# Optimization experiments

Hardware: AMD Instinct MI355X
Metric: run time of the kernel (lower is better)

The kernel has to match this reference:

```python
import jax, jax.numpy as jnp
import numpy as np

N = 50000
E = 800000
NFEAT = 128
HID = 64
EPS = 1e-5


def setup_inputs() -> dict:
    key = jax.random.key(0)
    ks = jax.random.split(key, 12)
    def xavier(k, fi, fo):
        lim = float(np.sqrt(6.0 / (fi + fo)))
        return jax.random.uniform(k, (fi, fo), jnp.float32, -lim, lim)
    return {
        "x": jax.random.normal(ks[0], (N, NFEAT), jnp.float32),
        "edge_index": jax.random.randint(ks[1], (2, E), 0, N),
        "W0": xavier(ks[2], NFEAT, HID), "b0": jnp.zeros((HID,), jnp.float32),
        "W1": xavier(ks[3], HID, HID),   "b1": jnp.zeros((HID,), jnp.float32),
        "W2": xavier(ks[4], HID, HID),   "b2": jnp.zeros((HID,), jnp.float32),
        "g0": jnp.ones((HID,), jnp.float32), "be0": jnp.zeros((HID,), jnp.float32),
        "g1": jnp.ones((HID,), jnp.float32), "be1": jnp.zeros((HID,), jnp.float32),
        "fcW": xavier(ks[5], HID, 1), "fcb": jnp.zeros((1,), jnp.float32),
    }


def _gcn_conv(h, src, dst, norm, W, b):
    # h: [N, Fin] -> transform then normalized scatter-add over edges (incl. self loops)
    m = (h @ W)[src] * norm[:, None]            # [E+N, Fout]
    return jax.ops.segment_sum(m, dst, num_segments=N) + b


def _batchnorm(h, g, b):
    mu = jnp.mean(h, axis=0)
    var = jnp.mean((h - mu) ** 2, axis=0)       # biased var, as torch BN
    return (h - mu) * jax.lax.rsqrt(var + EPS) * g + b


def reference(x, edge_index, W0, b0, W1, b1, W2, b2, g0, be0, g1, be1, fcW, fcb):
    loops = jnp.arange(N)
    src = jnp.concatenate([edge_index[0], loops])
    dst = jnp.concatenate([edge_index[1], loops])
    deg = jax.ops.segment_sum(jnp.ones_like(dst, jnp.float32), dst, num_segments=N)
    dinv = jnp.where(deg > 0, jax.lax.rsqrt(jnp.maximum(deg, 1.0)), 0.0)
    norm = dinv[src] * dinv[dst]                # symmetric GCN normalization

    h = x  # dropout is identity in eval
    h = jax.nn.relu(_batchnorm(_gcn_conv(h, src, dst, norm, W0, b0), g0, be0))
    h = jax.nn.relu(_batchnorm(_gcn_conv(h, src, dst, norm, W1, b1), g1, be1))
    h = jax.nn.relu(_gcn_conv(h, src, dst, norm, W2, b2))
    return (h @ fcW + fcb).squeeze(-1)          # [N]
```

## Files before the change

kernel.cpp:

```cpp
#include <hip/hip_runtime.h>

#define N_NODES 50000
#define N_EDGES 800000
#define NFEAT   128
#define HID     64
#define EPS_BN  1e-5f
#define NCHUNK  2
#define CHN     (N_NODES / NCHUNK)
#define SENT    50000

#define NPB     256
#define NCBIN   196
#define BPB     (NPB * NCHUNK)
#define EPBLK   2048
#define NB1     ((N_EDGES + EPBLK - 1) / EPBLK)
#define MAXPAD  (3 * BPB + 4)

#define NBINS   64
#define NBLKN   ((N_NODES + 255) / 256)
#define NPAIR   (N_NODES / 2)

typedef unsigned int   u32x4 __attribute__((ext_vector_type(4)));
typedef unsigned short u16x4 __attribute__((ext_vector_type(4)));

__device__ __forceinline__ float u2f_lo(unsigned int u) {
    union { unsigned int i; float f; } c; c.i = u << 16; return c.f;
}
__device__ __forceinline__ float u2f_hi(unsigned int u) {
    union { unsigned int i; float f; } c; c.i = u & 0xffff0000u; return c.f;
}
__device__ __forceinline__ float b2f(unsigned short u) {
    union { unsigned int i; float f; } c; c.i = ((unsigned int)u) << 16; return c.f;
}
__device__ __forceinline__ unsigned int f2b2(float lo, float hi) {
    union { float f; unsigned int i; } a, b;
    a.f = lo; b.f = hi;
    unsigned int x = (a.i + 0x7fffu + ((a.i >> 16) & 1u)) >> 16;
    unsigned int y = (b.i + 0x7fffu + ((b.i >> 16) & 1u)) & 0xffff0000u;
    return x | y;
}

__global__ void k_zero(float* __restrict__ st0, float* __restrict__ st1,
                       unsigned short* __restrict__ ts,
                       unsigned short* __restrict__ sent) {
    int i = threadIdx.x;
    if (i < 2 * HID) { st0[i] = 0.f; st1[i] = 0.f; }
    if (i < 32) ((unsigned int*)(ts + (size_t)N_NODES * HID))[i] = 0u;
    if (i < 4) sent[i] = SENT;
}

__global__ __launch_bounds__(256) void k_p1(const int* __restrict__ ei,
                                            unsigned int* __restrict__ packed,
                                            unsigned short* __restrict__ lrankE,
                                            int* __restrict__ bhE) {
    __shared__ int h[NCBIN];
    const int tid = threadIdx.x;
    for (int i = tid; i < NCBIN; i += 256) h[i] = 0;
    __syncthreads();
    const int base = blockIdx.x * EPBLK;
#pragma unroll
    for (int it = 0; it < EPBLK / 256; ++it) {
        int e = base + it * 256 + tid;
        if (e < N_EDGES) {
            unsigned s = (unsigned)ei[e];
            unsigned t = (unsigned)ei[N_EDGES + e];
            packed[e] = (t << 16) | s;
            lrankE[e] = (unsigned short)atomicAdd(&h[t >> 8], 1);
        }
    }
    __syncthreads();
    for (int i = tid; i < NCBIN; i += 256) bhE[i * NB1 + blockIdx.x] = h[i];
}

__global__ __launch_bounds__(512) void k_p1scan(int* __restrict__ bhE,
                                                int* __restrict__ bintotE) {
    const int b = blockIdx.x, tid = threadIdx.x;
    int v = (tid < NB1) ? bhE[b * NB1 + tid] : 0;
    __shared__ int sm[512];
    sm[tid] = v;
    __syncthreads();
    for (int off = 1; off < 512; off <<= 1) {
        int t = (tid >= off) ? sm[tid - off] : 0;
        __syncthreads();
        sm[tid] += t;
        __syncthreads();
    }
    if (tid < NB1) bhE[b * NB1 + tid] = sm[tid] - v;
    if (tid == 511) bintotE[b] = sm[511];
}

__global__ void k_binbase(const int* __restrict__ bintotE, int* __restrict__ binbase) {
    const int tid = threadIdx.x;
    int v = (tid < NCBIN) ? bintotE[tid] : 0;
    __shared__ int sm[256];
    sm[tid] = v;
    __syncthreads();
    for (int off = 1; off < 256; off <<= 1) {
        int t = (tid >= off) ? sm[tid - off] : 0;
        __syncthreads();
        sm[tid] += t;
        __syncthreads();
    }
    if (tid < NCBIN) binbase[tid] = sm[tid] - v;
    if (tid == NCBIN - 1) binbase[NCBIN] = sm[tid];
}

__global__ __launch_bounds__(256) void k_p3(const unsigned int* __restrict__ packed,
                                            const unsigned short* __restrict__ lrankE,
                                            const int* __restrict__ bhE,
                                            const int* __restrict__ binbase,
                                            unsigned int* __restrict__ binned) {
    const int base = blockIdx.x * EPBLK;
#pragma unroll
    for (int it = 0; it < EPBLK / 256; ++it) {
        int e = base + it * 256 + threadIdx.x;
        if (e < N_EDGES) {
            unsigned p = packed[e];
            int bin = (int)(p >> 24);
            int pos = binbase[bin] + bhE[bin * NB1 + blockIdx.x] + lrankE[e];
            binned[pos] = p;
        }
    }
}

__global__ __launch_bounds__(256) void k_p4(const unsigned int* __restrict__ binned,
                                            const int* __restrict__ binbase,
                                            unsigned short* __restrict__ col,
                                            int2* __restrict__ nspan,
                                            float* __restrict__ dinv) {
    __shared__ int cnt[BPB];
    __shared__ int lrp[BPB];
    __shared__ int fillc[BPB];
    __shared__ int scanTmp[256];
    const int bin = blockIdx.x, tid = threadIdx.x;
    const int e0 = binbase[bin], e1 = binbase[bin + 1];
    const int t0 = bin * NPB;
    for (int i = tid; i < BPB; i += 256) { cnt[i] = 0; fillc[i] = 0; }
    __syncthreads();
    for (int i = e0 + tid; i < e1; i += 256) {
        unsigned p = binned[i];
        int t = (int)(p >> 16), s = (int)(p & 0xffffu);
        int lb = ((t - t0) << 1) | (s >= CHN);
        atomicAdd(&cnt[lb], 1);
    }
    __syncthreads();
    const int p0 = (cnt[2 * tid] + 3) & ~3;
    const int p1 = (cnt[2 * tid + 1] + 3) & ~3;
    const int mysum = p0 + p1;
    scanTmp[tid] = mysum;
    __syncthreads();
    for (int off = 1; off < 256; off <<= 1) {
        int t = (tid >= off) ? scanTmp[tid - off] : 0;
        __syncthreads();
        scanTmp[tid] += t;
        __syncthreads();
    }
    const int pre = scanTmp[tid] - mysum;
    lrp[2 * tid]     = pre;
    lrp[2 * tid + 1] = pre + p0;
    const int colbase = ((e0 + 3) & ~3) + bin * MAXPAD;
    {
        const int node = t0 + tid;
        if (node < N_NODES) {
            int st = colbase + pre;
            nspan[node] = make_int2(st, st + p0 + p1);
            dinv[node] = rsqrtf((float)(cnt[2 * tid] + cnt[2 * tid + 1] + 1));
        }
    }
    __syncthreads();
    for (int i = e0 + tid; i < e1; i += 256) {
        unsigned p = binned[i];
        int t = (int)(p >> 16), s = (int)(p & 0xffffu);
        int lb = ((t - t0) << 1) | (s >= CHN);
        int pos = colbase + lrp[lb] + atomicAdd(&fillc[lb], 1);
        col[pos] = (unsigned short)s;
    }
    __syncthreads();
    for (int lb = tid; lb < BPB; lb += 256) {
        int c = cnt[lb];
        int pc = (c + 3) & ~3;
        int b2 = colbase + lrp[lb];
        for (int q = c; q < pc; ++q) col[b2 + q] = SENT;
    }
}

__device__ __forceinline__ int node_bin2(const int2* __restrict__ nspan, int i) {
    int iters = (nspan[i].y - nspan[i].x) >> 2;
    if (iters > NBINS - 1) iters = NBINS - 1;
    return (NBINS - 1) - iters;
}

__global__ __launch_bounds__(256) void k_hist2(const int2* __restrict__ nspan,
                                               int* __restrict__ bhistS,
                                               int* __restrict__ lrankS) {
    __shared__ int h[NBINS];
    const int tid = threadIdx.x;
    if (tid < NBINS) h[tid] = 0;
    __syncthreads();
    const int i = blockIdx.x * 256 + tid;
    if (i < N_NODES) lrankS[i] = atomicAdd(&h[node_bin2(nspan, i)], 1);
    __syncthreads();
    if (tid < NBINS) bhistS[tid * NBLKN + blockIdx.x] = h[tid];
}

__global__ __launch_bounds__(256) void k_colscan(int* __restrict__ bhistS,
                                                 int* __restrict__ bintotS) {
    const int b = blockIdx.x, tid = threadIdx.x;
    int v = (tid < NBLKN) ? bhistS[b * NBLKN + tid] : 0;
    __shared__ int sm[256];
    sm[tid] = v;
    __syncthreads();
    for (int off = 1; off < 256; off <<= 1) {
        int t = (tid >= off) ? sm[tid - off] : 0;
        __syncthreads();
        sm[tid] += t;
        __syncthreads();
    }
    if (tid < NBLKN) bhistS[b * NBLKN + tid] = sm[tid] - v;
    if (tid == 255) bintotS[b] = sm[255];
}

__global__ void k_binscan(const int* __restrict__ bintotS, int* __restrict__ binoffS) {
    int tid = threadIdx.x;
    int v = (tid < NBINS) ? bintotS[tid] : 0;
    int s = v;
#pragma unroll
    for (int off = 1; off < 64; off <<= 1) {
        int t = __shfl_up(s, off, 64);
        if (tid >= off) s += t;
    }
    if (tid < NBINS) binoffS[tid] = s - v;
}

__global__ __launch_bounds__(256) void k_sortscatter(const int2* __restrict__ nspan,
                                                     const int* __restrict__ binoffS,
                                                     const int* __restrict__ bhistS,
                                                     const int* __restrict__ lrankS,
                                                     int* __restrict__ perm,
                                                     int2* __restrict__ span) {
    int i = blockIdx.x * 256 + threadIdx.x;
    if (i >= N_NODES) return;
    int b = node_bin2(nspan, i);
    int pos = binoffS[b] + bhistS[b * NBLKN + blockIdx.x] + lrankS[i];
    perm[pos] = i;
    span[pos] = nspan[i];
}

template <int K, bool AFFINE, bool HBF16>
__global__ __launch_bounds__(256) void k_gemm(const void* __restrict__ Hv,
                                              const float* __restrict__ W,
                                              const float* __restrict__ dinv,
                                              const float* __restrict__ affine,
                                              unsigned short* __restrict__ ts) {
    __shared__ float Ws[K * HID];
    __shared__ float As[2 * K];
    const int tid = threadIdx.x;
    for (int i = tid * 4; i < K * HID; i += 256 * 4)
        *(float4*)&Ws[i] = *(const float4*)&W[i];
    if (AFFINE) {
        if (tid < (2 * K) / 4)
            *(float4*)&As[tid * 4] = *(const float4*)&affine[tid * 4];
    }
    __syncthreads();

    const int quad = tid & 3;
    const int rp_  = tid >> 2;
    const int row  = blockIdx.x * 128 + rp_ * 2;
    const int c0   = quad * 16;
    const bool v0  = row < N_NODES;
    const bool v1  = row + 1 < N_NODES;

    float acc0[16], acc1[16];
#pragma unroll
    for (int i = 0; i < 16; ++i) { acc0[i] = 0.f; acc1[i] = 0.f; }

    const float*          h0f = (const float*)Hv + (size_t)row * K;
    const unsigned short* h0b = (const unsigned short*)Hv + (size_t)row * K;
    const float4 z4 = make_float4(0.f, 0.f, 0.f, 0.f);

#pragma unroll 2
    for (int k = 0; k < K; k += 4) {
        float4 ha, hb;
        if constexpr (HBF16) {
            ushort4 ua = v0 ? *(const ushort4*)(h0b + k)     : make_ushort4(0, 0, 0, 0);
            ushort4 ub = v1 ? *(const ushort4*)(h0b + K + k) : make_ushort4(0, 0, 0, 0);
            ha = make_float4(b2f(ua.x), b2f(ua.y), b2f(ua.z), b2f(ua.w));
            hb = make_float4(b2f(ub.x), b2f(ub.y), b2f(ub.z), b2f(ub.w));
        } else {
            ha = v0 ? *(const float4*)(h0f + k)     : z4;
            hb = v1 ? *(const float4*)(h0f + K + k) : z4;
        }
        if (AFFINE) {
            const float4 sc = *(const float4*)&As[k];
            const float4 sh = *(const float4*)&As[K + k];
            ha.x = fmaxf(0.f, fmaf(ha.x, sc.x, sh.x));
            ha.y = fmaxf(0.f, fmaf(ha.y, sc.y, sh.y));
            ha.z = fmaxf(0.f, fmaf(ha.z, sc.z, sh.z));
            ha.w = fmaxf(0.f, fmaf(ha.w, sc.w, sh.w));
            hb.x = fmaxf(0.f, fmaf(hb.x, sc.x, sh.x));
            hb.y = fmaxf(0.f, fmaf(hb.y, sc.y, sh.y));
            hb.z = fmaxf(0.f, fmaf(hb.z, sc.z, sh.z));
            hb.w = fmaxf(0.f, fmaf(hb.w, sc.w, sh.w));
        }
        const float hA[4] = { ha.x, ha.y, ha.z, ha.w };
        const float hB[4] = { hb.x, hb.y, hb.z, hb.w };
#pragma unroll
        for (int j = 0; j < 4; ++j) {
            const float4* wr = (const float4*)&Ws[(k + j) * HID + c0];
            const float xa = hA[j], xb = hB[j];
#pragma unroll
            for (int q = 0; q < 4; ++q) {
                const float4 wv = wr[q];
                acc0[q * 4 + 0] = fmaf(xa, wv.x, acc0[q * 4 + 0]);
                acc0[q * 4 + 1] = fmaf(xa, wv.y, acc0[q * 4 + 1]);
                acc0[q * 4 + 2] = fmaf(xa, wv.z, acc0[q * 4 + 2]);
                acc0[q * 4 + 3] = fmaf(xa, wv.w, acc0[q * 4 + 3]);
                acc1[q * 4 + 0] = fmaf(xb, wv.x, acc1[q * 4 + 0]);
                acc1[q * 4 + 1] = fmaf(xb, wv.y, acc1[q * 4 + 1]);
                acc1[q * 4 + 2] = fmaf(xb, wv.z, acc1[q * 4 + 2]);
                acc1[q * 4 + 3] = fmaf(xb, wv.w, acc1[q * 4 + 3]);
            }
        }
    }

    if (v0) {
        const float d = dinv[row];
        uint4 p0, p1;
        p0.x = f2b2(acc0[0] * d,  acc0[1] * d);
        p0.y = f2b2(acc0[2] * d,  acc0[3] * d);
        p0.z = f2b2(acc0[4] * d,  acc0[5] * d);
        p0.w = f2b2(acc0[6] * d,  acc0[7] * d);
        p1.x = f2b2(acc0[8] * d,  acc0[9] * d);
        p1.y = f2b2(acc0[10] * d, acc0[11] * d);
        p1.z = f2b2(acc0[12] * d, acc0[13] * d);
        p1.w = f2b2(acc0[14] * d, acc0[15] * d);
        uint4* dst = (uint4*)&ts[(size_t)row * HID + c0];
        dst[0] = p0; dst[1] = p1;
    }
    if (v1) {
        const float d = dinv[row + 1];
        uint4 p0, p1;
        p0.x = f2b2(acc1[0] * d,  acc1[1] * d);
        p0.y = f2b2(acc1[2] * d,  acc1[3] * d);
        p0.z = f2b2(acc1[4] * d,  acc1[5] * d);
        p0.w = f2b2(acc1[6] * d,  acc1[7] * d);
        p1.x = f2b2(acc1[8] * d,  acc1[9] * d);
        p1.y = f2b2(acc1[10] * d, acc1[11] * d);
        p1.z = f2b2(acc1[12] * d, acc1[13] * d);
        p1.w = f2b2(acc1[14] * d, acc1[15] * d);
        uint4* dst = (uint4*)&ts[(size_t)(row + 1) * HID + c0];
        dst[0] = p0; dst[1] = p1;
    }
}

#define ACC8A(r)                                            \
    a0 += u2f_lo(r.x); a1 += u2f_hi(r.x);                   \
    a2 += u2f_lo(r.y); a3 += u2f_hi(r.y);                   \
    a4 += u2f_lo(r.z); a5 += u2f_hi(r.z);                   \
    a6 += u2f_lo(r.w); a7 += u2f_hi(r.w);
#define ACC8B(r)                                            \
    b0 += u2f_lo(r.x); b1 += u2f_hi(r.x);                   \
    b2 += u2f_lo(r.y); b3 += u2f_hi(r.y);                   \
    b4 += u2f_lo(r.z); b5 += u2f_hi(r.z);                   \
    b6 += u2f_lo(r.w); b7 += u2f_hi(r.w);

#define GATHER_PAIR(sA, sB)                                                     \
    {                                                                           \
        int eA = sA.x, eB = sB.x;                                               \
        const int endA = sA.y, endB = sB.y;                                     \
        const int lenA = endA - eA, lenB = endB - eB;                           \
        const int iters = (lenA > lenB ? lenA : lenB) >> 2;                     \
        u16x4 cA = __builtin_nontemporal_load((eA < endA) ? (const u16x4*)&col[eA] : (const u16x4*)sent4); \
        u16x4 cB = __builtin_nontemporal_load((eB < endB) ? (const u16x4*)&col[eB] : (const u16x4*)sent4); \
        for (int it = 0; it < iters; ++it) {                                    \
            eA += 4; eB += 4;                                                   \
            const u16x4 nA = __builtin_nontemporal_load((eA < endA) ? (const u16x4*)&col[eA] : (const u16x4*)sent4); \
            const u16x4 nB = __builtin_nontemporal_load((eB < endB) ? (const u16x4*)&col[eB] : (const u16x4*)sent4); \
            const uint4 rA0 = ts8[(size_t)cA.x * 8 + sl];                       \
            const uint4 rA1 = ts8[(size_t)cA.y * 8 + sl];                       \
            const uint4 rA2 = ts8[(size_t)cA.z * 8 + sl];                       \
            const uint4 rA3 = ts8[(size_t)cA.w * 8 + sl];                       \
            const uint4 rB0 = ts8[(size_t)cB.x * 8 + sl];                       \
            const uint4 rB1 = ts8[(size_t)cB.y * 8 + sl];                       \
            const uint4 rB2 = ts8[(size_t)cB.z * 8 + sl];                       \
            const uint4 rB3 = ts8[(size_t)cB.w * 8 + sl];                       \
            ACC8A(rA0) ACC8A(rA1) ACC8A(rA2) ACC8A(rA3)                         \
            ACC8B(rB0) ACC8B(rB1) ACC8B(rB2) ACC8B(rB3)                         \
            cA = nA; cB = nB;                                                   \
        }                                                                       \
    }

__global__ __launch_bounds__(256) void k_gather_bn(const uint4* __restrict__ ts8,
                                                   const int* __restrict__ perm,
                                                   const int2* __restrict__ span,
                                                   const unsigned short* __restrict__ col,
                                                   const unsigned short* __restrict__ sent4,
                                                   const float* __restrict__ dinv,
                                                   const float* __restrict__ bias,
                                                   unsigned short* __restrict__ y,
                                                   float* __restrict__ stats) {
    const int tid  = threadIdx.x;
    const int w    = tid >> 6;
    const int lane = tid & 63;
    const int grp  = lane >> 3;
    const int sl   = lane & 7;
    const float4 bv0 = ((const float4*)bias)[2 * sl];
    const float4 bv1 = ((const float4*)bias)[2 * sl + 1];
    float s0=0.f,s1=0.f,s2=0.f,s3=0.f,s4=0.f,s5=0.f,s6=0.f,s7=0.f;
    float q0=0.f,q1=0.f,q2=0.f,q3=0.f,q4=0.f,q5=0.f,q6=0.f,q7=0.f;

    for (int p = blockIdx.x * 32 + w * 8 + grp; p < NPAIR; p += gridDim.x * 32) {
        const int idxA = p;
        const int idxB = N_NODES - 1 - p;
        const int nodeA = perm[idxA];
        const int nodeB = perm[idxB];
        const int2 sA = span[idxA];
        const int2 sB = span[idxB];
        const uint4 selfA = ts8[(size_t)nodeA * 8 + sl];
        const uint4 selfB = ts8[(size_t)nodeB * 8 + sl];
        float a0 = u2f_lo(selfA.x), a1 = u2f_hi(selfA.x);
        float a2 = u2f_lo(selfA.y), a3 = u2f_hi(selfA.y);
        float a4 = u2f_lo(selfA.z), a5 = u2f_hi(selfA.z);
        float a6 = u2f_lo(selfA.w), a7 = u2f_hi(selfA.w);
        float b0 = u2f_lo(selfB.x), b1 = u2f_hi(selfB.x);
        float b2 = u2f_lo(selfB.y), b3 = u2f_hi(selfB.y);
        float b4 = u2f_lo(selfB.z), b5 = u2f_hi(selfB.z);
        float b6 = u2f_lo(selfB.w), b7 = u2f_hi(selfB.w);

        GATHER_PAIR(sA, sB)

        const float dA = dinv[nodeA];
        const float dB = dinv[nodeB];
        const float vA0 = fmaf(a0, dA, bv0.x), vA1 = fmaf(a1, dA, bv0.y);
        const float vA2 = fmaf(a2, dA, bv0.z), vA3 = fmaf(a3, dA, bv0.w);
        const float vA4 = fmaf(a4, dA, bv1.x), vA5 = fmaf(a5, dA, bv1.y);
        const float vA6 = fmaf(a6, dA, bv1.z), vA7 = fmaf(a7, dA, bv1.w);
        const float vB0 = fmaf(b0, dB, bv0.x), vB1 = fmaf(b1, dB, bv0.y);
        const float vB2 = fmaf(b2, dB, bv0.z), vB3 = fmaf(b3, dB, bv0.w);
        const float vB4 = fmaf(b4, dB, bv1.x), vB5 = fmaf(b5, dB, bv1.y);
        const float vB6 = fmaf(b6, dB, bv1.z), vB7 = fmaf(b7, dB, bv1.w);
        u32x4 yA, yB;
        yA.x = f2b2(vA0, vA1); yA.y = f2b2(vA2, vA3);
        yA.z = f2b2(vA4, vA5); yA.w = f2b2(vA6, vA7);
        yB.x = f2b2(vB0, vB1); yB.y = f2b2(vB2, vB3);
        yB.z = f2b2(vB4, vB5); yB.w = f2b2(vB6, vB7);
        __builtin_nontemporal_store(yA, (u32x4*)(y + (size_t)nodeA * HID + sl * 8));
        __builtin_nontemporal_store(yB, (u32x4*)(y + (size_t)nodeB * HID + sl * 8));
        s0 += vA0 + vB0; q0 += vA0 * vA0 + vB0 * vB0;
        s1 += vA1 + vB1; q1 += vA1 * vA1 + vB1 * vB1;
        s2 += vA2 + vB2; q2 += vA2 * vA2 + vB2 * vB2;
        s3 += vA3 + vB3; q3 += vA3 * vA3 + vB3 * vB3;
        s4 += vA4 + vB4; q4 += vA4 * vA4 + vB4 * vB4;
        s5 += vA5 + vB5; q5 += vA5 * vA5 + vB5 * vB5;
        s6 += vA6 + vB6; q6 += vA6 * vA6 + vB6 * vB6;
        s7 += vA7 + vB7; q7 += vA7 * vA7 + vB7 * vB7;
    }

#pragma unroll
    for (int off = 8; off <= 32; off <<= 1) {
        s0 += __shfl_xor(s0, off, 64); q0 += __shfl_xor(q0, off, 64);
        s1 += __shfl_xor(s1, off, 64); q1 += __shfl_xor(q1, off, 64);
        s2 += __shfl_xor(s2, off, 64); q2 += __shfl_xor(q2, off, 64);
        s3 += __shfl_xor(s3, off, 64); q3 += __shfl_xor(q3, off, 64);
        s4 += __shfl_xor(s4, off, 64); q4 += __shfl_xor(q4, off, 64);
        s5 += __shfl_xor(s5, off, 64); q5 += __shfl_xor(q5, off, 64);
        s6 += __shfl_xor(s6, off, 64); q6 += __shfl_xor(q6, off, 64);
        s7 += __shfl_xor(s7, off, 64); q7 += __shfl_xor(q7, off, 64);
    }
    __shared__ float smS[4][64];
    __shared__ float smQ[4][64];
    if (grp == 0) {
        *(float4*)&smS[w][8 * sl]     = make_float4(s0, s1, s2, s3);
        *(float4*)&smS[w][8 * sl + 4] = make_float4(s4, s5, s6, s7);
        *(float4*)&smQ[w][8 * sl]     = make_float4(q0, q1, q2, q3);
        *(float4*)&smQ[w][8 * sl + 4] = make_float4(q4, q5, q6, q7);
    }
    __syncthreads();
    if (tid < 64) {
        float t1 = smS[0][tid] + smS[1][tid] + smS[2][tid] + smS[3][tid];
        float t2 = smQ[0][tid] + smQ[1][tid] + smQ[2][tid] + smQ[3][tid];
        atomicAdd(&stats[tid],      t1);
        atomicAdd(&stats[64 + tid], t2);
    }
}

__global__ void k_bn_final(const float* __restrict__ stats,
                           const float* __restrict__ g,
                           const float* __restrict__ be,
                           float* __restrict__ affine) {
    int c = threadIdx.x;
    if (c < HID) {
        float mu  = stats[c] * (1.0f / N_NODES);
        float var = stats[64 + c] * (1.0f / N_NODES) - mu * mu;
        var = fmaxf(var, 0.f);
        float sc = g[c] * rsqrtf(var + EPS_BN);
        affine[c]       = sc;
        affine[HID + c] = fmaf(-mu, sc, be[c]);
    }
}

__global__ __launch_bounds__(256) void k_gather_final(const uint4* __restrict__ ts8,
                                                      const int* __restrict__ perm,
                                                      const int2* __restrict__ span,
                                                      const unsigned short* __restrict__ col,
                                                      const unsigned short* __restrict__ sent4,
                                                      const float* __restrict__ dinv,
                                                      const float* __restrict__ bias2,
                                                      const float* __restrict__ fcW,
                                                      const float* __restrict__ fcb,
                                                      float* __restrict__ out) {
    const int tid  = threadIdx.x;
    const int w    = tid >> 6;
    const int lane = tid & 63;
    const int grp  = lane >> 3;
    const int sl   = lane & 7;
    const float4 bv0 = ((const float4*)bias2)[2 * sl];
    const float4 bv1 = ((const float4*)bias2)[2 * sl + 1];
    const float4 fw0 = ((const float4*)fcW)[2 * sl];
    const float4 fw1 = ((const float4*)fcW)[2 * sl + 1];
    const float  fb  = fcb[0];

    for (int p = blockIdx.x * 32 + w * 8 + grp; p < NPAIR; p += gridDim.x * 32) {
        const int idxA = p;
        const int idxB = N_NODES - 1 - p;
        const int nodeA = perm[idxA];
        const int nodeB = perm[idxB];
        const int2 sA = span[idxA];
        const int2 sB = span[idxB];
        const uint4 selfA = ts8[(size_t)nodeA * 8 + sl];
        const uint4 selfB = ts8[(size_t)nodeB * 8 + sl];
        float a0 = u2f_lo(selfA.x), a1 = u2f_hi(selfA.x);
        float a2 = u2f_lo(selfA.y), a3 = u2f_hi(selfA.y);
        float a4 = u2f_lo(selfA.z), a5 = u2f_hi(selfA.z);
        float a6 = u2f_lo(selfA.w), a7 = u2f_hi(selfA.w);
        float b0 = u2f_lo(selfB.x), b1 = u2f_hi(selfB.x);
        float b2 = u2f_lo(selfB.y), b3 = u2f_hi(selfB.y);
        float b4 = u2f_lo(selfB.z), b5 = u2f_hi(selfB.z);
        float b6 = u2f_lo(selfB.w), b7 = u2f_hi(selfB.w);

        GATHER_PAIR(sA, sB)

        const float dA = dinv[nodeA];
        const float dB = dinv[nodeB];
        float vA = fmaxf(0.f, fmaf(a0, dA, bv0.x)) * fw0.x
                 + fmaxf(0.f, fmaf(a1, dA, bv0.y)) * fw0.y
                 + fmaxf(0.f, fmaf(a2, dA, bv0.z)) * fw0.z
                 + fmaxf(0.f, fmaf(a3, dA, bv0.w)) * fw0.w
                 + fmaxf(0.f, fmaf(a4, dA, bv1.x)) * fw1.x
                 + fmaxf(0.f, fmaf(a5, dA, bv1.y)) * fw1.y
                 + fmaxf(0.f, fmaf(a6, dA, bv1.z)) * fw1.z
                 + fmaxf(0.f, fmaf(a7, dA, bv1.w)) * fw1.w;
        float vB = fmaxf(0.f, fmaf(b0, dB, bv0.x)) * fw0.x
                 + fmaxf(0.f, fmaf(b1, dB, bv0.y)) * fw0.y
                 + fmaxf(0.f, fmaf(b2, dB, bv0.z)) * fw0.z
                 + fmaxf(0.f, fmaf(b3, dB, bv0.w)) * fw0.w
                 + fmaxf(0.f, fmaf(b4, dB, bv1.x)) * fw1.x
                 + fmaxf(0.f, fmaf(b5, dB, bv1.y)) * fw1.y
                 + fmaxf(0.f, fmaf(b6, dB, bv1.z)) * fw1.z
                 + fmaxf(0.f, fmaf(b7, dB, bv1.w)) * fw1.w;
#pragma unroll
        for (int off = 4; off >= 1; off >>= 1) {
            vA += __shfl_xor(vA, off, 64);
            vB += __shfl_xor(vB, off, 64);
        }
        if (sl == 0) {
            out[nodeA] = vA + fb;
            out[nodeB] = vB + fb;
        }
    }
}

extern "C" void kernel_launch(void* const* d_in, const int* in_sizes, int n_in,
                              void* d_out, int out_size, void* d_ws, size_t ws_size,
                              hipStream_t stream) {
    const float* x    = (const float*)d_in[0];
    const int*   ei   = (const int*)d_in[1];
    const float* W0   = (const float*)d_in[2];
    const float* b0   = (const float*)d_in[3];
    const float* W1   = (const float*)d_in[4];
    const float* b1   = (const float*)d_in[5];
    const float* W2   = (const float*)d_in[6];
    const float* b2   = (const float*)d_in[7];
    const float* g0   = (const float*)d_in[8];
    const float* be0  = (const float*)d_in[9];
    const float* g1   = (const float*)d_in[10];
    const float* be1  = (const float*)d_in[11];
    const float* fcW  = (const float*)d_in[12];
    const float* fcb  = (const float*)d_in[13];
    float* out        = (float*)d_out;

    char* ws = (char*)d_ws;
    size_t off = 0;
    auto alloc = [&](size_t bytes) -> void* {
        size_t o = off;
        off += (bytes + 255) & ~(size_t)255;
        return (void*)(ws + o);
    };
    unsigned short* ts   = (unsigned short*)alloc((size_t)(N_NODES + 1) * HID * 2);
    unsigned short* bufY = (unsigned short*)alloc((size_t)N_NODES * HID * 2);
    unsigned short* col  = (unsigned short*)alloc((size_t)(N_EDGES + NCBIN * MAXPAD + 16) * 2);
    unsigned int* packed = (unsigned int*)alloc((size_t)N_EDGES * 4);
    unsigned int* binned = (unsigned int*)alloc((size_t)N_EDGES * 4);
    unsigned short* lrankE = (unsigned short*)alloc((size_t)N_EDGES * 2);
    int*   bhE     = (int*)  alloc((size_t)NCBIN * NB1 * 4);
    int*   bintotE = (int*)  alloc((size_t)NCBIN * 4);
    int*   binbase = (int*)  alloc((size_t)(NCBIN + 1) * 4);
    int2*  nspan   = (int2*) alloc((size_t)N_NODES * 8);
    float* dinv    = (float*)alloc((size_t)N_NODES * 4);
    int*   perm    = (int*)  alloc((size_t)N_NODES * 4);
    int2*  span    = (int2*) alloc((size_t)N_NODES * 8);
    int*   lrankS  = (int*)  alloc((size_t)N_NODES * 4);
    int*   bhistS  = (int*)  alloc((size_t)NBINS * NBLKN * 4);
    int*   bintotS = (int*)  alloc((size_t)NBINS * 4);
    int*   binoffS = (int*)  alloc((size_t)NBINS * 4);
    unsigned short* sent = (unsigned short*)alloc(16);
    float* stats0  = (float*)alloc(2 * HID * 4);
    float* stats1  = (float*)alloc(2 * HID * 4);
    float* affine0 = (float*)alloc(2 * HID * 4);
    float* affine1 = (float*)alloc(2 * HID * 4);

    const int gGemm = (N_NODES + 127) / 128;
    const int gGath = (NPAIR + 31) / 32;

    k_zero<<<1, 256, 0, stream>>>(stats0, stats1, ts, sent);
    k_p1<<<NB1, 256, 0, stream>>>(ei, packed, lrankE, bhE);
    k_p1scan<<<NCBIN, 512, 0, stream>>>(bhE, bintotE);
    k_binbase<<<1, 256, 0, stream>>>(bintotE, binbase);
    k_p3<<<NB1, 256, 0, stream>>>(packed, lrankE, bhE, binbase, binned);
    k_p4<<<NCBIN, 256, 0, stream>>>(binned, binbase, col, nspan, dinv);
    k_hist2<<<NBLKN, 256, 0, stream>>>(nspan, bhistS, lrankS);
    k_colscan<<<NBINS, 256, 0, stream>>>(bhistS, bintotS);
    k_binscan<<<1, 64, 0, stream>>>(bintotS, binoffS);
    k_sortscatter<<<NBLKN, 256, 0, stream>>>(nspan, binoffS, bhistS, lrankS, perm, span);

    k_gemm<NFEAT, false, false><<<gGemm, 256, 0, stream>>>(x, W0, dinv, nullptr, ts);
    k_gather_bn<<<gGath, 256, 0, stream>>>((const uint4*)ts, perm, span, col, sent, dinv, b0, bufY, stats0);
    k_bn_final<<<1, 64, 0, stream>>>(stats0, g0, be0, affine0);

    k_gemm<HID, true, true><<<gGemm, 256, 0, stream>>>(bufY, W1, dinv, affine0, ts);
    k_gather_bn<<<gGath, 256, 0, stream>>>((const uint4*)ts, perm, span, col, sent, dinv, b1, bufY, stats1);
    k_bn_final<<<1, 64, 0, stream>>>(stats1, g1, be1, affine1);

    k_gemm<HID, true, true><<<gGemm, 256, 0, stream>>>(bufY, W2, dinv, affine1, ts);
    k_gather_final<<<gGath, 256, 0, stream>>>((const uint4*)ts, perm, span, col, sent, dinv, b2, fcW, fcb, out);
}
```

Measured before the change: 206.2 us.

## Split feature table into two 32-column planes and gather each half separately

The GEMM output table is stored as two separate bf16 planes of 32 features each, and every gather kernel runs twice, once per plane, with 8-byte loads instead of 16-byte loads. Each plane is half the size of the full table, so the randomly gathered working set is more likely to stay resident in cache. The cost is reading the edge column indices and spans twice and doubling the gather launches, and the final layer now does a read-modify-write on the output.

```diff
diff --git a/kernel.cpp b/kernel.cpp
--- a/kernel.cpp
+++ b/kernel.cpp
@@ -21,6 +21,7 @@
 #define NPAIR   (N_NODES / 2)
 
 typedef unsigned int   u32x4 __attribute__((ext_vector_type(4)));
+typedef unsigned int   u32x2 __attribute__((ext_vector_type(2)));
 typedef unsigned short u16x4 __attribute__((ext_vector_type(4)));
 
 __device__ __forceinline__ float u2f_lo(unsigned int u) {
@@ -41,11 +42,13 @@
 }
 
 __global__ void k_zero(float* __restrict__ st0, float* __restrict__ st1,
-                       unsigned short* __restrict__ ts,
+                       unsigned short* __restrict__ ts0,
+                       unsigned short* __restrict__ ts1,
                        unsigned short* __restrict__ sent) {
     int i = threadIdx.x;
     if (i < 2 * HID) { st0[i] = 0.f; st1[i] = 0.f; }
-    if (i < 32) ((unsigned int*)(ts + (size_t)N_NODES * HID))[i] = 0u;
+    if (i < 16) ((unsigned int*)(ts0 + (size_t)SENT * 32))[i] = 0u;
+    if (i < 16) ((unsigned int*)(ts1 + (size_t)SENT * 32))[i] = 0u;
     if (i < 4) sent[i] = SENT;
 }
 
@@ -251,7 +254,8 @@
                                               const float* __restrict__ W,
                                               const float* __restrict__ dinv,
                                               const float* __restrict__ affine,
-                                              unsigned short* __restrict__ ts) {
+                                              unsigned short* __restrict__ ts0,
+                                              unsigned short* __restrict__ ts1) {
     __shared__ float Ws[K * HID];
     __shared__ float As[2 * K];
     const int tid = threadIdx.x;
@@ -323,6 +327,8 @@
         }
     }
 
+    unsigned short* plane = (c0 < 32) ? ts0 : ts1;
+    const int pc0 = c0 & 31;
     if (v0) {
         const float d = dinv[row];
         uint4 p0, p1;
@@ -334,7 +340,7 @@
         p1.y = f2b2(acc0[10] * d, acc0[11] * d);
         p1.z = f2b2(acc0[12] * d, acc0[13] * d);
         p1.w = f2b2(acc0[14] * d, acc0[15] * d);
-        uint4* dst = (uint4*)&ts[(size_t)row * HID + c0];
+        uint4* dst = (uint4*)&plane[(size_t)row * 32 + pc0];
         dst[0] = p0; dst[1] = p1;
     }
     if (v1) {
@@ -348,23 +354,19 @@
         p1.y = f2b2(acc1[10] * d, acc1[11] * d);
         p1.z = f2b2(acc1[12] * d, acc1[13] * d);
         p1.w = f2b2(acc1[14] * d, acc1[15] * d);
-        uint4* dst = (uint4*)&ts[(size_t)(row + 1) * HID + c0];
+        uint4* dst = (uint4*)&plane[(size_t)(row + 1) * 32 + pc0];
         dst[0] = p0; dst[1] = p1;
     }
 }
 
-#define ACC8A(r)                                            \
+#define ACC4A(r)                                            \
     a0 += u2f_lo(r.x); a1 += u2f_hi(r.x);                   \
-    a2 += u2f_lo(r.y); a3 += u2f_hi(r.y);                   \
-    a4 += u2f_lo(r.z); a5 += u2f_hi(r.z);                   \
-    a6 += u2f_lo(r.w); a7 += u2f_hi(r.w);
-#define ACC8B(r)                                            \
+    a2 += u2f_lo(r.y); a3 += u2f_hi(r.y);
+#define ACC4B(r)                                            \
     b0 += u2f_lo(r.x); b1 += u2f_hi(r.x);                   \
-    b2 += u2f_lo(r.y); b3 += u2f_hi(r.y);                   \
-    b4 += u2f_lo(r.z); b5 += u2f_hi(r.z);                   \
-    b6 += u2f_lo(r.w); b7 += u2f_hi(r.w);
-
-#define GATHER_PAIR(sA, sB)                                                     \
+    b2 += u2f_lo(r.y); b3 += u2f_hi(r.y);
+
+#define GATHER_PAIR_H(sA, sB)                                                   \
     {                                                                           \
         int eA = sA.x, eB = sB.x;                                               \
         const int endA = sA.y, endB = sB.y;                                     \
@@ -376,38 +378,38 @@
             eA += 4; eB += 4;                                                   \
             const u16x4 nA = __builtin_nontemporal_load((eA < endA) ? (const u16x4*)&col[eA] : (const u16x4*)sent4); \
             const u16x4 nB = __builtin_nontemporal_load((eB < endB) ? (const u16x4*)&col[eB] : (const u16x4*)sent4); \
-            const uint4 rA0 = ts8[(size_t)cA.x * 8 + sl];                       \
-            const uint4 rA1 = ts8[(size_t)cA.y * 8 + sl];                       \
-            const uint4 rA2 = ts8[(size_t)cA.z * 8 + sl];                       \
-            const uint4 rA3 = ts8[(size_t)cA.w * 8 + sl];                       \
-            const uint4 rB0 = ts8[(size_t)cB.x * 8 + sl];                       \
-            const uint4 rB1 = ts8[(size_t)cB.y * 8 + sl];                       \
-            const uint4 rB2 = ts8[(size_t)cB.z * 8 + sl];                       \
-            const uint4 rB3 = ts8[(size_t)cB.w * 8 + sl];                       \
-            ACC8A(rA0) ACC8A(rA1) ACC8A(rA2) ACC8A(rA3)                         \
-            ACC8B(rB0) ACC8B(rB1) ACC8B(rB2) ACC8B(rB3)                         \
+            const uint2 rA0 = tsh[(size_t)cA.x * 8 + sl];                       \
+            const uint2 rA1 = tsh[(size_t)cA.y * 8 + sl];                       \
+            const uint2 rA2 = tsh[(size_t)cA.z * 8 + sl];                       \
+            const uint2 rA3 = tsh[(size_t)cA.w * 8 + sl];                       \
+            const uint2 rB0 = tsh[(size_t)cB.x * 8 + sl];                       \
+            const uint2 rB1 = tsh[(size_t)cB.y * 8 + sl];                       \
+            const uint2 rB2 = tsh[(size_t)cB.z * 8 + sl];                       \
+            const uint2 rB3 = tsh[(size_t)cB.w * 8 + sl];                       \
+            ACC4A(rA0) ACC4A(rA1) ACC4A(rA2) ACC4A(rA3)                         \
+            ACC4B(rB0) ACC4B(rB1) ACC4B(rB2) ACC4B(rB3)                         \
             cA = nA; cB = nB;                                                   \
         }                                                                       \
     }
 
-__global__ __launch_bounds__(256) void k_gather_bn(const uint4* __restrict__ ts8,
-                                                   const int* __restrict__ perm,
-                                                   const int2* __restrict__ span,
-                                                   const unsigned short* __restrict__ col,
-                                                   const unsigned short* __restrict__ sent4,
-                                                   const float* __restrict__ dinv,
-                                                   const float* __restrict__ bias,
-                                                   unsigned short* __restrict__ y,
-                                                   float* __restrict__ stats) {
+template <int HALF>
+__global__ __launch_bounds__(256) void k_gather_bn_h(const uint2* __restrict__ tsh,
+                                                     const int* __restrict__ perm,
+                                                     const int2* __restrict__ span,
+                                                     const unsigned short* __restrict__ col,
+                                                     const unsigned short* __restrict__ sent4,
+                                                     const float* __restrict__ dinv,
+                                                     const float* __restrict__ bias,
+                                                     unsigned short* __restrict__ y,
+                                                     float* __restrict__ stats) {
     const int tid  = threadIdx.x;
     const int w    = tid >> 6;
     const int lane = tid & 63;
     const int grp  = lane >> 3;
     const int sl   = lane & 7;
-    const float4 bv0 = ((const float4*)bias)[2 * sl];
-    const float4 bv1 = ((const float4*)bias)[2 * sl + 1];
-    float s0=0.f,s1=0.f,s2=0.f,s3=0.f,s4=0.f,s5=0.f,s6=0.f,s7=0.f;
-    float q0=0.f,q1=0.f,q2=0.f,q3=0.f,q4=0.f,q5=0.f,q6=0.f,q7=0.f;
+    const float4 bv = ((const float4*)(bias + HALF * 32))[sl];
+    float s0=0.f,s1=0.f,s2=0.f,s3=0.f;
+    float q0=0.f,q1=0.f,q2=0.f,q3=0.f;
 
     for (int p = blockIdx.x * 32 + w * 8 + grp; p < NPAIR; p += gridDim.x * 32) {
         const int idxA = p;
@@ -416,44 +418,30 @@
         const int nodeB = perm[idxB];
         const int2 sA = span[idxA];
         const int2 sB = span[idxB];
-        const uint4 selfA = ts8[(size_t)nodeA * 8 + sl];
-        const uint4 selfB = ts8[(size_t)nodeB * 8 + sl];
+        const uint2 selfA = tsh[(size_t)nodeA * 8 + sl];
+        const uint2 selfB = tsh[(size_t)nodeB * 8 + sl];
         float a0 = u2f_lo(selfA.x), a1 = u2f_hi(selfA.x);
         float a2 = u2f_lo(selfA.y), a3 = u2f_hi(selfA.y);
-        float a4 = u2f_lo(selfA.z), a5 = u2f_hi(selfA.z);
-        float a6 = u2f_lo(selfA.w), a7 = u2f_hi(selfA.w);
         float b0 = u2f_lo(selfB.x), b1 = u2f_hi(selfB.x);
         float b2 = u2f_lo(selfB.y), b3 = u2f_hi(selfB.y);
-        float b4 = u2f_lo(selfB.z), b5 = u2f_hi(selfB.z);
-        float b6 = u2f_lo(selfB.w), b7 = u2f_hi(selfB.w);
-
-        GATHER_PAIR(sA, sB)
+
+        GATHER_PAIR_H(sA, sB)
 
         const float dA = dinv[nodeA];
         const float dB = dinv[nodeB];
-        const float vA0 = fmaf(a0, dA, bv0.x), vA1 = fmaf(a1, dA, bv0.y);
-        const float vA2 = fmaf(a2, dA, bv0.z), vA3 = fmaf(a3, dA, bv0.w);
-        const float vA4 = fmaf(a4, dA, bv1.x), vA5 = fmaf(a5, dA, bv1.y);
-        const float vA6 = fmaf(a6, dA, bv1.z), vA7 = fmaf(a7, dA, bv1.w);
-        const float vB0 = fmaf(b0, dB, bv0.x), vB1 = fmaf(b1, dB, bv0.y);
-        const float vB2 = fmaf(b2, dB, bv0.z), vB3 = fmaf(b3, dB, bv0.w);
-        const float vB4 = fmaf(b4, dB, bv1.x), vB5 = fmaf(b5, dB, bv1.y);
-        const float vB6 = fmaf(b6, dB, bv1.z), vB7 = fmaf(b7, dB, bv1.w);
-        u32x4 yA, yB;
+        const float vA0 = fmaf(a0, dA, bv.x), vA1 = fmaf(a1, dA, bv.y);
+        const float vA2 = fmaf(a2, dA, bv.z), vA3 = fmaf(a3, dA, bv.w);
+        const float vB0 = fmaf(b0, dB, bv.x), vB1 = fmaf(b1, dB, bv.y);
+        const float vB2 = fmaf(b2, dB, bv.z), vB3 = fmaf(b3, dB, bv.w);
+        u32x2 yA, yB;
         yA.x = f2b2(vA0, vA1); yA.y = f2b2(vA2, vA3);
-        yA.z = f2b2(vA4, vA5); yA.w = f2b2(vA6, vA7);
         yB.x = f2b2(vB0, vB1); yB.y = f2b2(vB2, vB3);
-        yB.z = f2b2(vB4, vB5); yB.w = f2b2(vB6, vB7);
-        __builtin_nontemporal_store(yA, (u32x4*)(y + (size_t)nodeA * HID + sl * 8));
-        __builtin_nontemporal_store(yB, (u32x4*)(y + (size_t)nodeB * HID + sl * 8));
+        __builtin_nontemporal_store(yA, (u32x2*)(y + (size_t)nodeA * HID + HALF * 32 + sl * 4));
+        __builtin_nontemporal_store(yB, (u32x2*)(y + (size_t)nodeB * HID + HALF * 32 + sl * 4));
         s0 += vA0 + vB0; q0 += vA0 * vA0 + vB0 * vB0;
         s1 += vA1 + vB1; q1 += vA1 * vA1 + vB1 * vB1;
         s2 += vA2 + vB2; q2 += vA2 * vA2 + vB2 * vB2;
         s3 += vA3 + vB3; q3 += vA3 * vA3 + vB3 * vB3;
-        s4 += vA4 + vB4; q4 += vA4 * vA4 + vB4 * vB4;
-        s5 += vA5 + vB5; q5 += vA5 * vA5 + vB5 * vB5;
-        s6 += vA6 + vB6; q6 += vA6 * vA6 + vB6 * vB6;
-        s7 += vA7 + vB7; q7 += vA7 * vA7 + vB7 * vB7;
     }
 
 #pragma unroll
@@ -462,25 +450,19 @@
         s1 += __shfl_xor(s1, off, 64); q1 += __shfl_xor(q1, off, 64);
         s2 += __shfl_xor(s2, off, 64); q2 += __shfl_xor(q2, off, 64);
         s3 += __shfl_xor(s3, off, 64); q3 += __shfl_xor(q3, off, 64);
-        s4 += __shfl_xor(s4, off, 64); q4 += __shfl_xor(q4, off, 64);
-        s5 += __shfl_xor(s5, off, 64); q5 += __shfl_xor(q5, off, 64);
-        s6 += __shfl_xor(s6, off, 64); q6 += __shfl_xor(q6, off, 64);
-        s7 += __shfl_xor(s7, off, 64); q7 += __shfl_xor(q7, off, 64);
-    }
-    __shared__ float smS[4][64];
-    __shared__ float smQ[4][64];
+    }
+    __shared__ float smS[4][32];
+    __shared__ float smQ[4][32];
     if (grp == 0) {
-        *(float4*)&smS[w][8 * sl]     = make_float4(s0, s1, s2, s3);
-        *(float4*)&smS[w][8 * sl + 4] = make_float4(s4, s5, s6, s7);
-        *(float4*)&smQ[w][8 * sl]     = make_float4(q0, q1, q2, q3);
-        *(float4*)&smQ[w][8 * sl + 4] = make_float4(q4, q5, q6, q7);
-    }
-    __syncthreads();
-    if (tid < 64) {
+        *(float4*)&smS[w][4 * sl] = make_float4(s0, s1, s2, s3);
+        *(float4*)&smQ[w][4 * sl] = make_float4(q0, q1, q2, q3);
+    }
+    __syncthreads();
+    if (tid < 32) {
         float t1 = smS[0][tid] + smS[1][tid] + smS[2][tid] + smS[3][tid];
         float t2 = smQ[0][tid] + smQ[1][tid] + smQ[2][tid] + smQ[3][tid];
-        atomicAdd(&stats[tid],      t1);
-        atomicAdd(&stats[64 + tid], t2);
+        atomicAdd(&stats[HALF * 32 + tid],      t1);
+        atomicAdd(&stats[64 + HALF * 32 + tid], t2);
     }
 }
 
@@ -499,26 +481,25 @@
     }
 }
 
-__global__ __launch_bounds__(256) void k_gather_final(const uint4* __restrict__ ts8,
-                                                      const int* __restrict__ perm,
-                                                      const int2* __restrict__ span,
-                                                      const unsigned short* __restrict__ col,
-                                                      const unsigned short* __restrict__ sent4,
-                                                      const float* __restrict__ dinv,
-                                                      const float* __restrict__ bias2,
-                                                      const float* __restrict__ fcW,
-                                                      const float* __restrict__ fcb,
-                                                      float* __restrict__ out) {
+template <int HALF>
+__global__ __launch_bounds__(256) void k_gather_final_h(const uint2* __restrict__ tsh,
+                                                        const int* __restrict__ perm,
+                                                        const int2* __restrict__ span,
+                                                        const unsigned short* __restrict__ col,
+                                                        const unsigned short* __restrict__ sent4,
+                                                        const float* __restrict__ dinv,
+                                                        const float* __restrict__ bias2,
+                                                        const float* __restrict__ fcW,
+                                                        const float* __restrict__ fcb,
+                                                        float* __restrict__ out) {
     const int tid  = threadIdx.x;
     const int w    = tid >> 6;
     const int lane = tid & 63;
     const int grp  = lane >> 3;
     const int sl   = lane & 7;
-    const float4 bv0 = ((const float4*)bias2)[2 * sl];
-    const float4 bv1 = ((const float4*)bias2)[2 * sl + 1];
-    const float4 fw0 = ((const float4*)fcW)[2 * sl];
-    const float4 fw1 = ((const float4*)fcW)[2 * sl + 1];
-    const float  fb  = fcb[0];
+    const float4 bv = ((const float4*)(bias2 + HALF * 32))[sl];
+    const float4 fw = ((const float4*)(fcW  + HALF * 32))[sl];
+    const float  fb = fcb[0];
 
     for (int p = blockIdx.x * 32 + w * 8 + grp; p < NPAIR; p += gridDim.x * 32) {
         const int idxA = p;
@@ -527,45 +508,38 @@
         const int nodeB = perm[idxB];
         const int2 sA = span[idxA];
         const int2 sB = span[idxB];
-        const uint4 selfA = ts8[(size_t)nodeA * 8 + sl];
-        const uint4 selfB = ts8[(size_t)nodeB * 8 + sl];
+        const uint2 selfA = tsh[(size_t)nodeA * 8 + sl];
+        const uint2 selfB = tsh[(size_t)nodeB * 8 + sl];
         float a0 = u2f_lo(selfA.x), a1 = u2f_hi(selfA.x);
         float a2 = u2f_lo(selfA.y), a3 = u2f_hi(selfA.y);
-        float a4 = u2f_lo(selfA.z), a5 = u2f_hi(selfA.z);
-        float a6 = u2f_lo(selfA.w), a7 = u2f_hi(selfA.w);
         float b0 = u2f_lo(selfB.x), b1 = u2f_hi(selfB.x);
         float b2 = u2f_lo(selfB.y), b3 = u2f_hi(selfB.y);
-        float b4 = u2f_lo(selfB.z), b5 = u2f_hi(selfB.z);
-        float b6 = u2f_lo(selfB.w), b7 = u2f_hi(selfB.w);
-
-        GATHER_PAIR(sA, sB)
+
+        GATHER_PAIR_H(sA, sB)
 
         const float dA = dinv[nodeA];
         const float dB = dinv[nodeB];
-        float vA = fmaxf(0.f, fmaf(a0, dA, bv0.x)) * fw0.x
-                 + fmaxf(0.f, fmaf(a1, dA, bv0.y)) * fw0.y
-                 + fmaxf(0.f, fmaf(a2, dA, bv0.z)) * fw0.z
-                 + fmaxf(0.f, fmaf(a3, dA, bv0.w)) * fw0.w
-                 + fmaxf(0.f, fmaf(a4, dA, bv1.x)) * fw1.x
-                 + fmaxf(0.f, fmaf(a5, dA, bv1.y)) * fw1.y
-                 + fmaxf(0.f, fmaf(a6, dA, bv1.z)) * fw1.z
-                 + fmaxf(0.f, fmaf(a7, dA, bv1.w)) * fw1.w;
-        float vB = fmaxf(0.f, fmaf(b0, dB, bv0.x)) * fw0.x
-                 + fmaxf(0.f, fmaf(b1, dB, bv0.y)) * fw0.y
-                 + fmaxf(0.f, fmaf(b2, dB, bv0.z)) * fw0.z
-                 + fmaxf(0.f, fmaf(b3, dB, bv0.w)) * fw0.w
-                 + fmaxf(0.f, fmaf(b4, dB, bv1.x)) * fw1.x
-                 + fmaxf(0.f, fmaf(b5, dB, bv1.y)) * fw1.y
-                 + fmaxf(0.f, fmaf(b6, dB, bv1.z)) * fw1.z
-                 + fmaxf(0.f, fmaf(b7, dB, bv1.w)) * fw1.w;
+        float vA = fmaxf(0.f, fmaf(a0, dA, bv.x)) * fw.x
+                 + fmaxf(0.f, fmaf(a1, dA, bv.y)) * fw.y
+                 + fmaxf(0.f, fmaf(a2, dA, bv.z)) * fw.z
+                 + fmaxf(0.f, fmaf(a3, dA, bv.w)) * fw.w;
+        float vB = fmaxf(0.f, fmaf(b0, dB, bv.x)) * fw.x
+                 + fmaxf(0.f, fmaf(b1, dB, bv.y)) * fw.y
+                 + fmaxf(0.f, fmaf(b2, dB, bv.z)) * fw.z
+                 + fmaxf(0.f, fmaf(b3, dB, bv.w)) * fw.w;
 #pragma unroll
         for (int off = 4; off >= 1; off >>= 1) {
             vA += __shfl_xor(vA, off, 64);
             vB += __shfl_xor(vB, off, 64);
         }
         if (sl == 0) {
-            out[nodeA] = vA + fb;
-            out[nodeB] = vB + fb;
+            if (HALF == 0) {
+                out[nodeA] = vA + fb;
+                out[nodeB] = vB + fb;
+            } else {
+                out[nodeA] += vA;
+                out[nodeB] += vB;
+            }
         }
     }
 }
@@ -596,7 +570,8 @@
         off += (bytes + 255) & ~(size_t)255;
         return (void*)(ws + o);
     };
-    unsigned short* ts   = (unsigned short*)alloc((size_t)(N_NODES + 1) * HID * 2);
+    unsigned short* ts0  = (unsigned short*)alloc((size_t)(N_NODES + 1) * 32 * 2);
+    unsigned short* ts1  = (unsigned short*)alloc((size_t)(N_NODES + 1) * 32 * 2);
     unsigned short* bufY = (unsigned short*)alloc((size_t)N_NODES * HID * 2);
     unsigned short* col  = (unsigned short*)alloc((size_t)(N_EDGES + NCBIN * MAXPAD + 16) * 2);
     unsigned int* packed = (unsigned int*)alloc((size_t)N_EDGES * 4);
@@ -622,7 +597,7 @@
     const int gGemm = (N_NODES + 127) / 128;
     const int gGath = (NPAIR + 31) / 32;
 
-    k_zero<<<1, 256, 0, stream>>>(stats0, stats1, ts, sent);
+    k_zero<<<1, 256, 0, stream>>>(stats0, stats1, ts0, ts1, sent);
     k_p1<<<NB1, 256, 0, stream>>>(ei, packed, lrankE, bhE);
     k_p1scan<<<NCBIN, 512, 0, stream>>>(bhE, bintotE);
     k_binbase<<<1, 256, 0, stream>>>(bintotE, binbase);
@@ -633,14 +608,17 @@
     k_binscan<<<1, 64, 0, stream>>>(bintotS, binoffS);
     k_sortscatter<<<NBLKN, 256, 0, stream>>>(nspan, binoffS, bhistS, lrankS, perm, span);
 
-    k_gemm<NFEAT, false, false><<<gGemm, 256, 0, stream>>>(x, W0, dinv, nullptr, ts);
-    k_gather_bn<<<gGath, 256, 0, stream>>>((const uint4*)ts, perm, span, col, sent, dinv, b0, bufY, stats0);
+    k_gemm<NFEAT, false, false><<<gGemm, 256, 0, stream>>>(x, W0, dinv, nullptr, ts0, ts1);
+    k_gather_bn_h<0><<<gGath, 256, 0, stream>>>((const uint2*)ts0, perm, span, col, sent, dinv, b0, bufY, stats0);
+    k_gather_bn_h<1><<<gGath, 256, 0, stream>>>((const uint2*)ts1, perm, span, col, sent, dinv, b0, bufY, stats0);
     k_bn_final<<<1, 64, 0, stream>>>(stats0, g0, be0, affine0);
 
-    k_gemm<HID, true, true><<<gGemm, 256, 0, stream>>>(bufY, W1, dinv, affine0, ts);
-    k_gather_bn<<<gGath, 256, 0, stream>>>((const uint4*)ts, perm, span, col, sent, dinv, b1, bufY, stats1);
+    k_gemm<HID, true, true><<<gGemm, 256, 0, stream>>>(bufY, W1, dinv, affine0, ts0, ts1);
+    k_gather_bn_h<0><<<gGath, 256, 0, stream>>>((const uint2*)ts0, perm, span, col, sent, dinv, b1, bufY, stats1);
+    k_gather_bn_h<1><<<gGath, 256, 0, stream>>>((const uint2*)ts1, perm, span, col, sent, dinv, b1, bufY, stats1);
     k_bn_final<<<1, 64, 0, stream>>>(stats1, g1, be1, affine1);
 
-    k_gemm<HID, true, true><<<gGemm, 256, 0, stream>>>(bufY, W2, dinv, affine1, ts);
-    k_gather_final<<<gGath, 256, 0, stream>>>((const uint4*)ts, perm, span, col, sent, dinv, b2, fcW, fcb, out);
-}
+    k_gemm<HID, true, true><<<gGemm, 256, 0, stream>>>(bufY, W2, dinv, affine1, ts0, ts1);
+    k_gather_final_h<0><<<gGath, 256, 0, stream>>>((const uint2*)ts0, perm, span, col, sent, dinv, b2, fcW, fcb, out);
+    k_gather_final_h<1><<<gGath, 256, 0, stream>>>((const uint2*)ts1, perm, span, col, sent, dinv, b2, fcW, fcb, out);
+}
```

New measurement: 243.8 us. +18.2%, slower.
